# Kernel tuning notes

Hardware: AMD Instinct MI355X
Metric: run time of the kernel (lower is better)

## Reference

```python
import jax, jax.numpy as jnp
import numpy as np

P = 7  # pool_size (module fast path: pool_size=7, C=512)


def setup_inputs() -> dict:
    key = jax.random.key(0)
    B, N, H, W, C = 2, 64, 38, 38, 512
    k1, k2, k3, k4, k5 = jax.random.split(key, 5)
    feature_map = jax.random.normal(k1, (B, H, W, C), dtype=jnp.float32)
    # ROI = (y, x, h, w) in integer feature-map coordinates, h,w >= P so every
    # pooling cell is non-empty and the bin boundaries partition the ROI exactly
    # (the original's max(size,1) clamp is then a no-op).
    h = jax.random.randint(k2, (B, N), P, H + 1, dtype=jnp.int32)
    w = jax.random.randint(k3, (B, N), P, W + 1, dtype=jnp.int32)
    y = jnp.floor(jax.random.uniform(k4, (B, N)) * (H - h + 1).astype(jnp.float32)).astype(jnp.int32)
    x = jnp.floor(jax.random.uniform(k5, (B, N)) * (W - w + 1).astype(jnp.float32)).astype(jnp.int32)
    rois = jnp.stack([y, x, h, w], axis=-1)
    return {"feature_map": feature_map, "rois": rois}


def _roi_pool(feature_map, rois, pool_size=P):
    # feature_map: [B,H,W,C] float, rois: [B,N,4] int (y, x, h, w)
    B, H, W, C = feature_map.shape
    N = rois.shape[1]
    PP = pool_size * pool_size
    y0 = rois[..., 0][:, :, None]  # [B,N,1]
    x0 = rois[..., 1][:, :, None]
    h = rois[..., 2][:, :, None]
    w = rois[..., 3][:, :, None]

    # For a pixel at relative row r inside an ROI of height h (h >= pool_size),
    # its bin b is the largest b with floor(b*h/pool_size) <= r, i.e.
    # b = (pool_size*r + pool_size-1) // h  -- identical to the original's
    # [floor(b*h/P), floor((b+1)*h/P)) partition (last bin end = h).
    rel_y = jnp.arange(H, dtype=jnp.int32)[None, None, :] - y0  # [B,N,H]
    rel_x = jnp.arange(W, dtype=jnp.int32)[None, None, :] - x0  # [B,N,W]
    ybin = (pool_size * rel_y + (pool_size - 1)) // jnp.maximum(h, 1)
    xbin = (pool_size * rel_x + (pool_size - 1)) // jnp.maximum(w, 1)
    valid_y = (rel_y >= 0) & (rel_y < h)  # [B,N,H]
    valid_x = (rel_x >= 0) & (rel_x < w)  # [B,N,W]

    cell = ybin[:, :, :, None] * pool_size + xbin[:, :, None, :]  # [B,N,H,W]
    valid = valid_y[:, :, :, None] & valid_x[:, :, None, :]
    cell = jnp.where(valid, cell, PP)  # PP = dump cell for out-of-ROI pixels

    roi_id = jnp.arange(B * N, dtype=jnp.int32).reshape(B, N, 1, 1)
    seg = (roi_id * (PP + 1) + cell).reshape(-1)  # [B*N*H*W]

    # Values: feature map broadcast over the ROI axis -> one fused segment-max.
    vals = jnp.broadcast_to(feature_map[:, None], (B, N, H, W, C)).reshape(-1, C)
    pooled = jax.ops.segment_max(vals, seg, num_segments=B * N * (PP + 1))
    pooled = pooled.reshape(B, N, PP + 1, C)[:, :, :PP]  # drop dump cell
    return pooled.reshape(B, N, pool_size, pool_size, C)


def reference(feature_map, rois):
    return _roi_pool(feature_map, rois)
```

## Files before the change

### kernel.cpp

```cpp
#include <hip/hip_runtime.h>
#include <hip/hip_bf16.h>
#include <math.h>

#define RB 2
#define RN 64
#define RH 38
#define RW 38
#define RC 512
#define RP 7
#define CELLS (RB * RN * RP * RP)
#define CPI (RN * RP * RP)
#define PPI (CPI / 2)

typedef float vfloat4 __attribute__((ext_vector_type(4)));

__global__ __launch_bounds__(128) void roi_pool_kernel(
    const float* __restrict__ fm, const int* __restrict__ rois,
    float* __restrict__ out) {
  int wave = threadIdx.x >> 6;
  int lane = threadIdx.x & 63;

  int bx = blockIdx.x;
  int x = bx & 7;
  int j = bx >> 3;
  int img = x >> 2;
  int pair = img * PPI + ((j << 2) | (x & 3));
  int cell = pair * 2 + wave;

  int px = cell % RP;
  int t = cell / RP;
  int py = t % RP;
  t /= RP;
  int b = t / RN;

  const int* r = rois + (t << 2);
  int y0 = r[0], x0 = r[1], h = r[2], w = r[3];

  int ys = (py * h) / RP, ye = ((py + 1) * h) / RP;
  int xs = (px * w) / RP, xe = ((px + 1) * w) / RP;
  int bw = xe - xs;
  int cnt = bw * (ye - ys);

  const float4* p =
      (const float4*)(fm +
                      (size_t)((b * RH + y0 + ys) * RW + x0 + xs) * RC) +
      lane;
  const int pixstep = RC / 4;
  const int wrapstep = (RW - bw) * (RC / 4);

  float4 m0 = make_float4(-INFINITY, -INFINITY, -INFINITY, -INFINITY);
  float4 m1 = m0;

  float4 a0 = p[0];
  float4 a1 = p[64];
  int xrem = bw;
  for (int k = 1; k < cnt; ++k) {
    p += pixstep;
    if (--xrem == 0) { xrem = bw; p += wrapstep; }
    float4 n0 = p[0];
    float4 n1 = p[64];
    m0.x = fmaxf(m0.x, a0.x); m0.y = fmaxf(m0.y, a0.y);
    m0.z = fmaxf(m0.z, a0.z); m0.w = fmaxf(m0.w, a0.w);
    m1.x = fmaxf(m1.x, a1.x); m1.y = fmaxf(m1.y, a1.y);
    m1.z = fmaxf(m1.z, a1.z); m1.w = fmaxf(m1.w, a1.w);
    a0 = n0; a1 = n1;
  }
  m0.x = fmaxf(m0.x, a0.x); m0.y = fmaxf(m0.y, a0.y);
  m0.z = fmaxf(m0.z, a0.z); m0.w = fmaxf(m0.w, a0.w);
  m1.x = fmaxf(m1.x, a1.x); m1.y = fmaxf(m1.y, a1.y);
  m1.z = fmaxf(m1.z, a1.z); m1.w = fmaxf(m1.w, a1.w);

  vfloat4* o = (vfloat4*)(out + (size_t)cell * RC) + lane;
  vfloat4 s0 = {m0.x, m0.y, m0.z, m0.w};
  vfloat4 s1 = {m1.x, m1.y, m1.z, m1.w};
  __builtin_nontemporal_store(s0, o);
  __builtin_nontemporal_store(s1, o + 64);
}

extern "C" void kernel_launch(void* const* d_in, const int* in_sizes, int n_in,
                              void* d_out, int out_size, void* d_ws, size_t ws_size,
                              hipStream_t stream) {
  const float* fm = (const float*)d_in[0];
  const int* rois = (const int*)d_in[1];
  float* out = (float*)d_out;

  roi_pool_kernel<<<CELLS / 2, 128, 0, stream>>>(fm, rois, out);
}
```

Measured before the change: 69.55 us.

## Precompute 2x2 max pyramid and cover ROI bins with overlapping windows

Adds a pre-pass kernel that writes a 2x2 sliding-window max of the feature map into workspace. The ROI pool kernel then covers each bin (when at least 2x2) with overlapping 2x2 windows from this map, cutting per-bin loads roughly fourfold. Small bins fall back to direct reads. ROI fields are read via readfirstlane as scalars. The cost is an extra kernel launch and a full read and write of the feature map.

Measured after the change: 73.25 us. 5.3% more time.

```diff
diff --git a/kernel.cpp b/kernel.cpp
--- a/kernel.cpp
+++ b/kernel.cpp
@@ -11,12 +11,48 @@
 #define CELLS (RB * RN * RP * RP)
 #define CPI (RN * RP * RP)
 #define PPI (CPI / 2)
+#define C4 (RC / 4)
+#define NPIX (RB * RH * RW)
+#define STRIPS 5
+#define SLEN 8
 
 typedef float vfloat4 __attribute__((ext_vector_type(4)));
 
+__device__ __forceinline__ float4 max4(float4 a, float4 b) {
+  return make_float4(fmaxf(a.x, b.x), fmaxf(a.y, b.y), fmaxf(a.z, b.z),
+                     fmaxf(a.w, b.w));
+}
+
+__global__ __launch_bounds__(128) void pyr_kernel(
+    const float* __restrict__ fm, float* __restrict__ mhv) {
+  int sb = blockIdx.x;
+  int st = sb % STRIPS;
+  int t = sb / STRIPS;
+  int y = t % RH;
+  int b = t / RH;
+  int x0 = st * SLEN;
+  int len = min(SLEN, RW - x0);
+  int y1 = min(y + 1, RH - 1);
+  int lane = threadIdx.x;
+
+  const float4* f = (const float4*)fm;
+  const float4* r0 = f + ((size_t)((b * RH + y) * RW + x0)) * C4 + lane;
+  const float4* r1 = f + ((size_t)((b * RH + y1) * RW + x0)) * C4 + lane;
+  float4* o = (float4*)mhv + ((size_t)((b * RH + y) * RW + x0)) * C4 + lane;
+
+  float4 vprev = max4(r0[0], r1[0]);
+  for (int dx = 1; dx <= len; ++dx) {
+    int col = min(x0 + dx, RW - 1);
+    size_t off = (size_t)(col - x0) * C4;
+    float4 v = max4(r0[off], r1[off]);
+    o[(size_t)(dx - 1) * C4] = max4(vprev, v);
+    vprev = v;
+  }
+}
+
 __global__ __launch_bounds__(128) void roi_pool_kernel(
-    const float* __restrict__ fm, const int* __restrict__ rois,
-    float* __restrict__ out) {
+    const float* __restrict__ fm, const float* __restrict__ mhv,
+    const int* __restrict__ rois, float* __restrict__ out) {
   int wave = threadIdx.x >> 6;
   int lane = threadIdx.x & 63;
 
@@ -34,41 +70,48 @@
   int b = t / RN;
 
   const int* r = rois + (t << 2);
-  int y0 = r[0], x0 = r[1], h = r[2], w = r[3];
+  int y0 = __builtin_amdgcn_readfirstlane(r[0]);
+  int x0 = __builtin_amdgcn_readfirstlane(r[1]);
+  int h = __builtin_amdgcn_readfirstlane(r[2]);
+  int w = __builtin_amdgcn_readfirstlane(r[3]);
 
   int ys = (py * h) / RP, ye = ((py + 1) * h) / RP;
   int xs = (px * w) / RP, xe = ((px + 1) * w) / RP;
-  int bw = xe - xs;
-  int cnt = bw * (ye - ys);
-
-  const float4* p =
-      (const float4*)(fm +
-                      (size_t)((b * RH + y0 + ys) * RW + x0 + xs) * RC) +
-      lane;
-  const int pixstep = RC / 4;
-  const int wrapstep = (RW - bw) * (RC / 4);
+  int bh = ye - ys, bw = xe - xs;
 
   float4 m0 = make_float4(-INFINITY, -INFINITY, -INFINITY, -INFINITY);
   float4 m1 = m0;
 
-  float4 a0 = p[0];
-  float4 a1 = p[64];
-  int xrem = bw;
-  for (int k = 1; k < cnt; ++k) {
-    p += pixstep;
-    if (--xrem == 0) { xrem = bw; p += wrapstep; }
-    float4 n0 = p[0];
-    float4 n1 = p[64];
-    m0.x = fmaxf(m0.x, a0.x); m0.y = fmaxf(m0.y, a0.y);
-    m0.z = fmaxf(m0.z, a0.z); m0.w = fmaxf(m0.w, a0.w);
-    m1.x = fmaxf(m1.x, a1.x); m1.y = fmaxf(m1.y, a1.y);
-    m1.z = fmaxf(m1.z, a1.z); m1.w = fmaxf(m1.w, a1.w);
-    a0 = n0; a1 = n1;
+  if (bh >= 2 && bw >= 2) {
+    int ny = (bh + 1) >> 1, nx = (bw + 1) >> 1;
+    for (int iy = 0; iy < ny; ++iy) {
+      int yy = min(ys + 2 * iy, ye - 2);
+      const float4* rowp = (const float4*)mhv +
+                           ((size_t)((b * RH + y0 + yy) * RW + x0)) * C4 +
+                           lane;
+      for (int ix = 0; ix < nx; ++ix) {
+        int xx = min(xs + 2 * ix, xe - 2);
+        const float4* p = rowp + (size_t)xx * C4;
+        float4 v0 = p[0];
+        float4 v1 = p[64];
+        m0 = max4(m0, v0);
+        m1 = max4(m1, v1);
+      }
+    }
+  } else {
+    for (int yy = ys; yy < ye; ++yy) {
+      const float4* rowp = (const float4*)fm +
+                           ((size_t)((b * RH + y0 + yy) * RW + x0 + xs)) * C4 +
+                           lane;
+      for (int xx = 0; xx < bw; ++xx) {
+        float4 v0 = rowp[0];
+        float4 v1 = rowp[64];
+        m0 = max4(m0, v0);
+        m1 = max4(m1, v1);
+        rowp += C4;
+      }
+    }
   }
-  m0.x = fmaxf(m0.x, a0.x); m0.y = fmaxf(m0.y, a0.y);
-  m0.z = fmaxf(m0.z, a0.z); m0.w = fmaxf(m0.w, a0.w);
-  m1.x = fmaxf(m1.x, a1.x); m1.y = fmaxf(m1.y, a1.y);
-  m1.z = fmaxf(m1.z, a1.z); m1.w = fmaxf(m1.w, a1.w);
 
   vfloat4* o = (vfloat4*)(out + (size_t)cell * RC) + lane;
   vfloat4 s0 = {m0.x, m0.y, m0.z, m0.w};
@@ -83,6 +126,8 @@
   const float* fm = (const float*)d_in[0];
   const int* rois = (const int*)d_in[1];
   float* out = (float*)d_out;
+  float* mhv = (float*)d_ws;
 
-  roi_pool_kernel<<<CELLS / 2, 128, 0, stream>>>(fm, rois, out);
+  pyr_kernel<<<RB * RH * STRIPS, 128, 0, stream>>>(fm, mhv);
+  roi_pool_kernel<<<CELLS / 2, 128, 0, stream>>>(fm, mhv, rois, out);
 }
```
